# Kernel optimization log

Hardware: AMD Instinct MI355X
Metric: run time of the kernel (lower is better)

Reference implementation:

```python
import jax, jax.numpy as jnp
import numpy as np

RESO = 128
CB_BITS = 4
NUM_FEAT = 2 ** CB_BITS  # 16
DATA_DIM = 16
RADIUS = 1.3
MLP_W = 128
NFREQ = 4
PE_DIM = NFREQ * 3 * 2  # 24
BATCH = 1024
STEP = RADIUS / RESO
N_INTR = int(1.732 * RADIUS * 2 / STEP)  # 443 boundary samples
NS = N_INTR - 1                           # 442 intervals / sample points

NBR = jnp.array([[0,0,0],[0,0,1],[0,1,0],[0,1,1],[1,0,0],[1,0,1],[1,1,0],[1,1,1]], dtype=jnp.int32)


def expand_bits(v):
    v = (v * jnp.uint32(65537)) & jnp.uint32(4278190335)
    v = (v * jnp.uint32(257)) & jnp.uint32(251719695)
    v = (v * jnp.uint32(17)) & jnp.uint32(3272356035)
    v = (v * jnp.uint32(5)) & jnp.uint32(1227133513)
    return v


def morton3d(x, y, z):
    return expand_bits(x) | (expand_bits(y) << 1) | (expand_bits(z) << 2)


def pos_encode(d, nfreq):
    freqs = 2.0 ** jnp.arange(nfreq, dtype=d.dtype)          # [F]
    ang = d[..., None, :] * freqs[:, None]                   # [..., F, 3]
    pe = jnp.concatenate([jnp.sin(ang), jnp.cos(ang)], -1)   # [..., F, 6]
    return pe.reshape(*d.shape[:-1], nfreq * 6)


def setup_inputs() -> dict:
    key = jax.random.key(0)
    ks = jax.random.split(key, 8)
    rays_o = (jax.random.uniform(ks[0], (BATCH, 3), jnp.float32) - 0.5) * RADIUS
    d = jax.random.normal(ks[1], (BATCH, 3), jnp.float32)
    rays_d = d / jnp.linalg.norm(d, axis=-1, keepdims=True)
    grid = 0.01 * jax.random.normal(ks[2], (RESO ** 3, NUM_FEAT), jnp.float32)
    codebook = 0.1 * jax.random.normal(ks[3], (NUM_FEAT, DATA_DIM), jnp.float32)
    in_dim = DATA_DIM + PE_DIM
    b1s = 1.0 / np.sqrt(in_dim)
    b2s = 1.0 / np.sqrt(MLP_W)
    W1 = jax.random.uniform(ks[4], (in_dim, MLP_W), jnp.float32, -b1s, b1s)
    b1 = jax.random.uniform(ks[5], (MLP_W,), jnp.float32, -b1s, b1s)
    W2 = jax.random.uniform(ks[6], (MLP_W, 4), jnp.float32, -b2s, b2s)
    b2 = jax.random.uniform(ks[7], (4,), jnp.float32, -b2s, b2s)
    return {"rays_o": rays_o, "rays_d": rays_d, "grid": grid, "codebook": codebook,
            "W1": W1, "b1": b1, "W2": W2, "b2": b2, "level": 0}


def _forward(rays_o, rays_d, grid, codebook, W1, b1, W2, b2):
    # --- get_intersections: ray/AABB entry, uniform marching ---
    safe_d = jnp.where(jnp.abs(rays_d) < 1e-8, 1e-8, rays_d)
    t_a = (-RADIUS - rays_o) / safe_d
    t_b = (RADIUS - rays_o) / safe_d
    tmin = jnp.max(jnp.minimum(t_a, t_b), axis=-1)
    tmax = jnp.min(jnp.maximum(t_a, t_b), axis=-1)
    tnear = jnp.maximum(tmin, 0.0)
    intrs = tnear[:, None] + jnp.arange(N_INTR, dtype=jnp.float32) * STEP  # [B, N_INTR]
    tmid = 0.5 * (intrs[:, :-1] + intrs[:, 1:])                            # [B, NS]
    pts = rays_o[:, None, :] + rays_d[:, None, :] * tmid[..., None]        # [B, NS, 3]
    mask = (tmid < tmax[:, None]) & jnp.all(jnp.abs(pts) <= RADIUS, -1)    # [B, NS]

    # --- normalize to grid coords ---
    p = (pts / RADIUS + 1.0) * (RESO / 2.0)                                # [B, NS, 3]
    tl = jnp.floor(p)
    off = p - tl                                                           # [B, NS, 3]
    nbr = jnp.clip(tl.astype(jnp.int32)[:, :, None, :] + NBR, 0, RESO - 1) # [B, NS, 8, 3]
    idx = morton3d(nbr[..., 0].astype(jnp.uint32), nbr[..., 1].astype(jnp.uint32),
                   nbr[..., 2].astype(jnp.uint32)).astype(jnp.int32)       # [B, NS, 8]

    # --- straight-through VQ codebook lookup ---
    feat_soft = jax.nn.softmax(grid[idx], axis=-1)                         # [B, NS, 8, F]
    hard_idx = jnp.argmax(feat_soft, axis=-1)
    feat_hard = jax.nn.one_hot(hard_idx, NUM_FEAT, dtype=feat_soft.dtype)
    feat = feat_hard - jax.lax.stop_gradient(feat_soft) + feat_soft
    data = jnp.einsum('bsnf,fd->bsnd', feat, codebook)                     # [B, NS, 8, D]

    # --- trilinear interpolation over 8 corners ---
    w = jnp.prod(NBR * off[:, :, None, :] + (1 - NBR) * (1.0 - off[:, :, None, :]), -1)
    data_interp = jnp.einsum('bsn,bsnd->bsd', w, data)                     # [B, NS, D]

    # --- renderer MLP ---
    dir_pe = pos_encode(rays_d, NFREQ)                                     # [B, 24]
    dir_pe = jnp.broadcast_to(dir_pe[:, None, :], (rays_d.shape[0], NS, PE_DIM))
    x = jnp.concatenate([data_interp, dir_pe], -1)                         # [B, NS, 40]
    h = jax.nn.relu(jnp.einsum('bsi,io->bso', x, W1) + b1)
    preact = jnp.einsum('bsi,io->bso', h, W2) + b2                         # [B, NS, 4]
    density = jnp.where(mask, jax.nn.relu(preact[..., 0]), 0.0)            # masked_scatter
    color_raw = jnp.where(mask[..., None], preact[..., 1:], 0.0)

    # --- sigma2alpha + shrgb2rgb compositing ---
    delta = (intrs[:, 1:] - intrs[:, :-1]) * jnp.linalg.norm(rays_d, axis=-1, keepdims=True)
    alpha = 1.0 - jnp.exp(-density * delta)                                # [B, NS]
    T = jnp.cumprod(1.0 - alpha + 1e-10, axis=1)
    T = jnp.concatenate([jnp.ones_like(T[:, :1]), T[:, :-1]], axis=1)      # exclusive
    abs_light = alpha * T                                                  # weights
    rgb = jnp.sum(abs_light[..., None] * jax.nn.sigmoid(color_raw), axis=1)
    rgb = rgb + (1.0 - jnp.sum(abs_light, axis=1))[:, None]                # white bkgd
    return rgb, alpha


def reference(rays_o, rays_d, grid, codebook, W1, b1, W2, b2, level):
    assert level == 0
    return _forward(rays_o, rays_d, grid, codebook, W1, b1, W2, b2)
```

## Files before the change

### kernel.cpp

```cpp
#include <hip/hip_runtime.h>
#include <math.h>
#include <stdint.h>

#define RESO 128
#define NUM_FEAT 16
#define DATA_DIM 16
#define MLP_W 128
#define NFREQ 4
#define BATCH 1024
#define NS 442
#define NT 384
#define NWAVES 6
#define STEPF ((float)(1.3 / 128.0))

typedef __attribute__((ext_vector_type(8))) short short8;
typedef __attribute__((ext_vector_type(4))) float f32x4;
typedef __attribute__((ext_vector_type(4))) int int4v;

static __device__ __forceinline__ unsigned short f2bf(float f) {
    union { float f; uint32_t u; } v; v.f = f;
    uint32_t r = v.u + 0x7FFFu + ((v.u >> 16) & 1u);
    return (unsigned short)(r >> 16);
}
static __device__ __forceinline__ uint32_t pack2bf(float a, float b) {
    return (uint32_t)f2bf(a) | ((uint32_t)f2bf(b) << 16);
}

static __device__ __forceinline__ uint32_t expand_bits(uint32_t v) {
    v = (v * 65537u) & 4278190335u;
    v = (v * 257u)   & 251719695u;
    v = (v * 17u)    & 3272356035u;
    v = (v * 5u)     & 1227133513u;
    return v;
}
static __device__ __forceinline__ uint32_t morton3d(uint32_t x, uint32_t y, uint32_t z) {
    return expand_bits(x) | (expand_bits(y) << 1) | (expand_bits(z) << 2);
}

__global__ __launch_bounds__(NT) void nerf_main_kernel(
    const float* __restrict__ rays_o, const float* __restrict__ rays_d,
    const float* __restrict__ grid, const float* __restrict__ cbg,
    const float* __restrict__ W1g, const float* __restrict__ b1g,
    const float* __restrict__ W2g, const float* __restrict__ b2g,
    float* __restrict__ out_rgb, float* __restrict__ out_alpha) {

    __shared__ __align__(16) float cbs[NUM_FEAT * DATA_DIM];
    __shared__ __align__(16) float pe_b1s[MLP_W];
    __shared__ __align__(16) unsigned short W1pL[8 * 64 * 8];
    __shared__ float wtot[NWAVES];
    __shared__ float wred[NWAVES][4];

    const int b = blockIdx.x;
    const int t = threadIdx.x;
    const int wid = t >> 6;
    const int lane = t & 63;
    const int g = lane >> 4;

    const float o0 = rays_o[b * 3 + 0], o1 = rays_o[b * 3 + 1], o2 = rays_o[b * 3 + 2];
    const float d0 = rays_d[b * 3 + 0], d1 = rays_d[b * 3 + 1], d2 = rays_d[b * 3 + 2];
    const float R = 1.3f;
    float sd0 = (fabsf(d0) < 1e-8f) ? 1e-8f : d0;
    float sd1 = (fabsf(d1) < 1e-8f) ? 1e-8f : d1;
    float sd2 = (fabsf(d2) < 1e-8f) ? 1e-8f : d2;
    float ta0 = (-R - o0) / sd0, tb0 = (R - o0) / sd0;
    float ta1 = (-R - o1) / sd1, tb1 = (R - o1) / sd1;
    float ta2 = (-R - o2) / sd2, tb2 = (R - o2) / sd2;
    float tmin = fmaxf(fmaxf(fminf(ta0, tb0), fminf(ta1, tb1)), fminf(ta2, tb2));
    float tmax = fminf(fminf(fmaxf(ta0, tb0), fmaxf(ta1, tb1)), fmaxf(ta2, tb2));
    float tnear = fmaxf(tmin, 0.0f);
    float nrm = sqrtf(d0 * d0 + d1 * d1 + d2 * d2);

    if (t < NUM_FEAT * DATA_DIM) cbs[t] = cbg[t];

    for (int idx = t; idx < 8 * 64 * 8; idx += NT) {
        int j = idx & 7, l = (idx >> 3) & 63, mh = idx >> 9;
        int gg = l >> 4, col = l & 15;
        int k = gg * 8 + j;
        float v = (k < DATA_DIM) ? W1g[k * MLP_W + mh * 16 + col] : 0.0f;
        W1pL[idx] = f2bf(v);
    }

    if (t < MLP_W) {
        float acc = b1g[t];
#pragma unroll
        for (int f = 0; f < NFREQ; ++f) {
            float fr = (float)(1 << f);
            acc = fmaf(__sinf(d0 * fr), W1g[(DATA_DIM + f * 6 + 0) * MLP_W + t], acc);
            acc = fmaf(__sinf(d1 * fr), W1g[(DATA_DIM + f * 6 + 1) * MLP_W + t], acc);
            acc = fmaf(__sinf(d2 * fr), W1g[(DATA_DIM + f * 6 + 2) * MLP_W + t], acc);
            acc = fmaf(__cosf(d0 * fr), W1g[(DATA_DIM + f * 6 + 3) * MLP_W + t], acc);
            acc = fmaf(__cosf(d1 * fr), W1g[(DATA_DIM + f * 6 + 4) * MLP_W + t], acc);
            acc = fmaf(__cosf(d2 * fr), W1g[(DATA_DIM + f * 6 + 5) * MLP_W + t], acc);
        }
        pe_b1s[t] = acc;
    }
    __syncthreads();

    const int s = t;
    float i0 = tnear + (float)s * STEPF;
    float i1 = tnear + (float)(s + 1) * STEPF;
    float tm = 0.5f * (i0 + i1);
    float delta = (i1 - i0) * nrm;
    float px = o0 + d0 * tm, py = o1 + d1 * tm, pz = o2 + d2 * tm;
    bool m = (tm < tmax) && (fabsf(px) <= R) && (fabsf(py) <= R) && (fabsf(pz) <= R);

    float alpha = 0.0f, c0 = 0.0f, c1 = 0.0f, c2 = 0.0f;

    float x[DATA_DIM];
#pragma unroll
    for (int j = 0; j < DATA_DIM; ++j) x[j] = 0.0f;

    if (m) {
        float gx = (px / R + 1.0f) * (RESO * 0.5f);
        float gy = (py / R + 1.0f) * (RESO * 0.5f);
        float gz = (pz / R + 1.0f) * (RESO * 0.5f);
        float flx = floorf(gx), fly = floorf(gy), flz = floorf(gz);
        float ox = gx - flx, oy = gy - fly, oz = gz - flz;
        int ix = (int)flx, iy = (int)fly, iz = (int)flz;

#pragma unroll
        for (int n = 0; n < 8; ++n) {
            int bx = (n >> 2) & 1, by = (n >> 1) & 1, bz = n & 1;
            int cx = min(max(ix + bx, 0), RESO - 1);
            int cy = min(max(iy + by, 0), RESO - 1);
            int cz = min(max(iz + bz, 0), RESO - 1);
            uint32_t mi = morton3d((uint32_t)cx, (uint32_t)cy, (uint32_t)cz);
            float wv = (bx ? ox : 1.0f - ox) * (by ? oy : 1.0f - oy) * (bz ? oz : 1.0f - oz);

            const float4* g4 = (const float4*)(grid + ((size_t)mi << 4));
            float4 A = g4[0], B = g4[1], C = g4[2], D = g4[3];
            float v[16] = {A.x, A.y, A.z, A.w, B.x, B.y, B.z, B.w,
                           C.x, C.y, C.z, C.w, D.x, D.y, D.z, D.w};
            float bestv = v[0];
            int bi = 0;
#pragma unroll
            for (int j = 1; j < 16; ++j) {
                bi = (v[j] > bestv) ? j : bi;
                bestv = fmaxf(v[j], bestv);
            }

            const float4* cbr = (const float4*)&cbs[bi * DATA_DIM];
            float4 ca = cbr[0], cb4 = cbr[1], cc = cbr[2], cd = cbr[3];
            x[0]  = fmaf(wv, ca.x,  x[0]);  x[1]  = fmaf(wv, ca.y,  x[1]);
            x[2]  = fmaf(wv, ca.z,  x[2]);  x[3]  = fmaf(wv, ca.w,  x[3]);
            x[4]  = fmaf(wv, cb4.x, x[4]);  x[5]  = fmaf(wv, cb4.y, x[5]);
            x[6]  = fmaf(wv, cb4.z, x[6]);  x[7]  = fmaf(wv, cb4.w, x[7]);
            x[8]  = fmaf(wv, cc.x,  x[8]);  x[9]  = fmaf(wv, cc.y,  x[9]);
            x[10] = fmaf(wv, cc.z,  x[10]); x[11] = fmaf(wv, cc.w,  x[11]);
            x[12] = fmaf(wv, cd.x,  x[12]); x[13] = fmaf(wv, cd.y,  x[13]);
            x[14] = fmaf(wv, cd.z,  x[14]); x[15] = fmaf(wv, cd.w,  x[15]);
        }
    }

    if (__any((int)m)) {
        uint32_t wp[8];
#pragma unroll
        for (int i = 0; i < 8; ++i) wp[i] = pack2bf(x[2 * i], x[2 * i + 1]);

        short8 Bf[4];
#pragma unroll
        for (int ns = 0; ns < 4; ++ns) {
            int src = ns * 16 + (lane & 15);
            int v0a = __shfl((int)wp[0], src, 64), v0b = __shfl((int)wp[4], src, 64);
            int v1a = __shfl((int)wp[1], src, 64), v1b = __shfl((int)wp[5], src, 64);
            int v2a = __shfl((int)wp[2], src, 64), v2b = __shfl((int)wp[6], src, 64);
            int v3a = __shfl((int)wp[3], src, 64), v3b = __shfl((int)wp[7], src, 64);
            union { int4v i; short8 s; } u;
            u.i.x = (g == 0) ? v0a : (g == 1) ? v0b : 0;
            u.i.y = (g == 0) ? v1a : (g == 1) ? v1b : 0;
            u.i.z = (g == 0) ? v2a : (g == 1) ? v2b : 0;
            u.i.w = (g == 0) ? v3a : (g == 1) ? v3b : 0;
            Bf[ns] = u.s;
        }

        float p[4][4];
#pragma unroll
        for (int ns = 0; ns < 4; ++ns)
#pragma unroll
            for (int c = 0; c < 4; ++c) p[ns][c] = 0.0f;

        const int4v* Ap = (const int4v*)W1pL;
#pragma unroll
        for (int mh = 0; mh < 8; ++mh) {
            union { int4v i; short8 s; } ua;
            ua.i = Ap[mh * 64 + lane];
            short8 Af = ua.s;

            f32x4 bias = *(const f32x4*)&pe_b1s[mh * 16 + 4 * g];
            f32x4 accv[4];
            accv[0] = __builtin_amdgcn_mfma_f32_16x16x32_bf16(Af, Bf[0], bias, 0, 0, 0);
            accv[1] = __builtin_amdgcn_mfma_f32_16x16x32_bf16(Af, Bf[1], bias, 0, 0, 0);
            accv[2] = __builtin_amdgcn_mfma_f32_16x16x32_bf16(Af, Bf[2], bias, 0, 0, 0);
            accv[3] = __builtin_amdgcn_mfma_f32_16x16x32_bf16(Af, Bf[3], bias, 0, 0, 0);

            float4 w2r[4];
            w2r[0] = *(const float4*)(W2g + (mh * 16 + 4 * g + 0) * 4);
            w2r[1] = *(const float4*)(W2g + (mh * 16 + 4 * g + 1) * 4);
            w2r[2] = *(const float4*)(W2g + (mh * 16 + 4 * g + 2) * 4);
            w2r[3] = *(const float4*)(W2g + (mh * 16 + 4 * g + 3) * 4);
#pragma unroll
            for (int ns = 0; ns < 4; ++ns) {
#pragma unroll
                for (int r = 0; r < 4; ++r) {
                    float h = fmaxf(accv[ns][r], 0.0f);
                    float4 wr2 = w2r[r];
                    p[ns][0] = fmaf(h, wr2.x, p[ns][0]);
                    p[ns][1] = fmaf(h, wr2.y, p[ns][1]);
                    p[ns][2] = fmaf(h, wr2.z, p[ns][2]);
                    p[ns][3] = fmaf(h, wr2.w, p[ns][3]);
                }
            }
        }

#pragma unroll
        for (int ns = 0; ns < 4; ++ns)
#pragma unroll
            for (int c = 0; c < 4; ++c) {
                float v = p[ns][c];
                v += __shfl_xor(v, 16, 64);
                v += __shfl_xor(v, 32, 64);
                p[ns][c] = v;
            }

        float pre[4];
#pragma unroll
        for (int c = 0; c < 4; ++c) {
            float v = (g == 0) ? p[0][c] : (g == 1) ? p[1][c] : (g == 2) ? p[2][c] : p[3][c];
            pre[c] = v + b2g[c];
        }

        if (m) {
            float dens = fmaxf(pre[0], 0.0f);
            alpha = 1.0f - __expf(-dens * delta);
            c0 = 1.0f / (1.0f + __expf(-pre[1]));
            c1 = 1.0f / (1.0f + __expf(-pre[2]));
            c2 = 1.0f / (1.0f + __expf(-pre[3]));
        }
    }

    float inc = 1.0f - alpha + 1e-10f;
#pragma unroll
    for (int off = 1; off < 64; off <<= 1) {
        float u = __shfl_up(inc, off, 64);
        if (lane >= off) inc *= u;
    }
    float excl = __shfl_up(inc, 1, 64);
    if (lane == 0) excl = 1.0f;
    if (lane == 63) wtot[wid] = inc;
    __syncthreads();

    float wpre = 1.0f;
#pragma unroll
    for (int w = 0; w < NWAVES; ++w)
        if (w < wid) wpre *= wtot[w];
    float T = wpre * excl;
    float wgt = alpha * T;
    float r0 = wgt * c0, r1 = wgt * c1, r2 = wgt * c2, rw = wgt;

    out_alpha[b * NS + s] = alpha;
    if (t < NS - NT) out_alpha[b * NS + NT + t] = 0.0f;

#pragma unroll
    for (int off = 32; off >= 1; off >>= 1) {
        r0 += __shfl_down(r0, off, 64);
        r1 += __shfl_down(r1, off, 64);
        r2 += __shfl_down(r2, off, 64);
        rw += __shfl_down(rw, off, 64);
    }
    if (lane == 0) { wred[wid][0] = r0; wred[wid][1] = r1; wred[wid][2] = r2; wred[wid][3] = rw; }
    __syncthreads();
    if (t == 0) {
        float s0 = 0, s1 = 0, s2 = 0, sw = 0;
#pragma unroll
        for (int i = 0; i < NWAVES; ++i) {
            s0 += wred[i][0]; s1 += wred[i][1]; s2 += wred[i][2]; sw += wred[i][3];
        }
        float bg = 1.0f - sw;
        out_rgb[b * 3 + 0] = s0 + bg;
        out_rgb[b * 3 + 1] = s1 + bg;
        out_rgb[b * 3 + 2] = s2 + bg;
    }
}

extern "C" void kernel_launch(void* const* d_in, const int* in_sizes, int n_in,
                              void* d_out, int out_size, void* d_ws, size_t ws_size,
                              hipStream_t stream) {
    const float* rays_o   = (const float*)d_in[0];
    const float* rays_d   = (const float*)d_in[1];
    const float* grid     = (const float*)d_in[2];
    const float* codebook = (const float*)d_in[3];
    const float* W1       = (const float*)d_in[4];
    const float* b1       = (const float*)d_in[5];
    const float* W2       = (const float*)d_in[6];
    const float* b2       = (const float*)d_in[7];
    float* out = (float*)d_out;

    nerf_main_kernel<<<BATCH, NT, 0, stream>>>(
        rays_o, rays_d, grid, codebook, W1, b1, W2, b2,
        out , out + BATCH * 3 );
}
```

Before: 31.10 us.

## Split rays into 64-sample chunks per wave with separate combine kernel

Each wave now handles one 64-sample chunk of a ray (7 chunks per ray, 4 chunks per block), writing partial color, weight and transmittance to a workspace. A second small kernel composites the chunks in order. This removes the block-wide syncs for the cross-wave scan and reduction, and lets blocks or waves whose chunks lie entirely outside the volume skip the MLP and W1 staging. In exchange it adds a second launch, a workspace round trip, and per-wave recomputation of the positional-encoding bias.

```diff
diff --git a/kernel.cpp b/kernel.cpp
--- a/kernel.cpp
+++ b/kernel.cpp
@@ -9,8 +9,10 @@
 #define NFREQ 4
 #define BATCH 1024
 #define NS 442
-#define NT 384
-#define NWAVES 6
+#define NT 256
+#define CPR 7
+#define NENT (BATCH * CPR)
+#define NBLK (NENT / 4)
 #define STEPF ((float)(1.3 / 128.0))
 
 typedef __attribute__((ext_vector_type(8))) short short8;
@@ -42,19 +44,20 @@
     const float* __restrict__ grid, const float* __restrict__ cbg,
     const float* __restrict__ W1g, const float* __restrict__ b1g,
     const float* __restrict__ W2g, const float* __restrict__ b2g,
-    float* __restrict__ out_rgb, float* __restrict__ out_alpha) {
+    float* __restrict__ part, float* __restrict__ out_alpha) {
 
     __shared__ __align__(16) float cbs[NUM_FEAT * DATA_DIM];
-    __shared__ __align__(16) float pe_b1s[MLP_W];
     __shared__ __align__(16) unsigned short W1pL[8 * 64 * 8];
-    __shared__ float wtot[NWAVES];
-    __shared__ float wred[NWAVES][4];
-
-    const int b = blockIdx.x;
+    __shared__ __align__(16) float peb[4][MLP_W];
+
     const int t = threadIdx.x;
-    const int wid = t >> 6;
+    const int wslot = t >> 6;
     const int lane = t & 63;
     const int g = lane >> 4;
+
+    const int e = blockIdx.x * 4 + wslot;
+    const int b = e / CPR;
+    const int c = e - b * CPR;
 
     const float o0 = rays_o[b * 3 + 0], o1 = rays_o[b * 3 + 1], o2 = rays_o[b * 3 + 2];
     const float d0 = rays_d[b * 3 + 0], d1 = rays_d[b * 3 + 1], d2 = rays_d[b * 3 + 2];
@@ -70,39 +73,61 @@
     float tnear = fmaxf(tmin, 0.0f);
     float nrm = sqrtf(d0 * d0 + d1 * d1 + d2 * d2);
 
-    if (t < NUM_FEAT * DATA_DIM) cbs[t] = cbg[t];
-
-    for (int idx = t; idx < 8 * 64 * 8; idx += NT) {
-        int j = idx & 7, l = (idx >> 3) & 63, mh = idx >> 9;
-        int gg = l >> 4, col = l & 15;
-        int k = gg * 8 + j;
-        float v = (k < DATA_DIM) ? W1g[k * MLP_W + mh * 16 + col] : 0.0f;
-        W1pL[idx] = f2bf(v);
-    }
-
-    if (t < MLP_W) {
-        float acc = b1g[t];
-#pragma unroll
-        for (int f = 0; f < NFREQ; ++f) {
-            float fr = (float)(1 << f);
-            acc = fmaf(__sinf(d0 * fr), W1g[(DATA_DIM + f * 6 + 0) * MLP_W + t], acc);
-            acc = fmaf(__sinf(d1 * fr), W1g[(DATA_DIM + f * 6 + 1) * MLP_W + t], acc);
-            acc = fmaf(__sinf(d2 * fr), W1g[(DATA_DIM + f * 6 + 2) * MLP_W + t], acc);
-            acc = fmaf(__cosf(d0 * fr), W1g[(DATA_DIM + f * 6 + 3) * MLP_W + t], acc);
-            acc = fmaf(__cosf(d1 * fr), W1g[(DATA_DIM + f * 6 + 4) * MLP_W + t], acc);
-            acc = fmaf(__cosf(d2 * fr), W1g[(DATA_DIM + f * 6 + 5) * MLP_W + t], acc);
-        }
-        pe_b1s[t] = acc;
-    }
-    __syncthreads();
-
-    const int s = t;
+    const int s = c * 64 + lane;
     float i0 = tnear + (float)s * STEPF;
     float i1 = tnear + (float)(s + 1) * STEPF;
     float tm = 0.5f * (i0 + i1);
     float delta = (i1 - i0) * nrm;
     float px = o0 + d0 * tm, py = o1 + d1 * tm, pz = o2 + d2 * tm;
-    bool m = (tm < tmax) && (fabsf(px) <= R) && (fabsf(py) <= R) && (fabsf(pz) <= R);
+    bool m = (s < NS) && (tm < tmax) &&
+             (fabsf(px) <= R) && (fabsf(py) <= R) && (fabsf(pz) <= R);
+    const bool anym = __any((int)m);
+
+    int blkact = __syncthreads_or((int)anym);
+    if (blkact) {
+        if (t < NUM_FEAT * DATA_DIM) cbs[t] = cbg[t];
+        for (int idx = t; idx < 8 * 64 * 8; idx += NT) {
+            int j = idx & 7, l = (idx >> 3) & 63, mh = idx >> 9;
+            int k = (l >> 4) * 8 + j;
+            float v = (k < DATA_DIM) ? W1g[k * MLP_W + mh * 16 + (l & 15)] : 0.0f;
+            W1pL[idx] = f2bf(v);
+        }
+        __syncthreads();
+    }
+
+    if (!anym) {
+        if (s < NS) out_alpha[b * NS + s] = 0.0f;
+        if (lane == 0) {
+            float* P = part + (size_t)e * 8;
+            P[0] = 0.0f; P[1] = 0.0f; P[2] = 0.0f; P[3] = 0.0f; P[4] = 1.0f;
+        }
+        return;
+    }
+
+    {
+        float sn[NFREQ][3], cs[NFREQ][3];
+#pragma unroll
+        for (int f = 0; f < NFREQ; ++f) {
+            float fr = (float)(1 << f);
+            sn[f][0] = __sinf(d0 * fr); sn[f][1] = __sinf(d1 * fr); sn[f][2] = __sinf(d2 * fr);
+            cs[f][0] = __cosf(d0 * fr); cs[f][1] = __cosf(d1 * fr); cs[f][2] = __cosf(d2 * fr);
+        }
+        float a0 = b1g[lane], a1 = b1g[64 + lane];
+#pragma unroll
+        for (int f = 0; f < NFREQ; ++f) {
+#pragma unroll
+            for (int ax = 0; ax < 3; ++ax) {
+                const float* ws = &W1g[(DATA_DIM + f * 6 + ax) * MLP_W];
+                const float* wc = &W1g[(DATA_DIM + f * 6 + 3 + ax) * MLP_W];
+                a0 = fmaf(sn[f][ax], ws[lane], a0);
+                a1 = fmaf(sn[f][ax], ws[64 + lane], a1);
+                a0 = fmaf(cs[f][ax], wc[lane], a0);
+                a1 = fmaf(cs[f][ax], wc[64 + lane], a1);
+            }
+        }
+        peb[wslot][lane] = a0;
+        peb[wslot][64 + lane] = a1;
+    }
 
     float alpha = 0.0f, c0 = 0.0f, c1 = 0.0f, c2 = 0.0f;
 
@@ -152,7 +177,7 @@
         }
     }
 
-    if (__any((int)m)) {
+    {
         uint32_t wp[8];
 #pragma unroll
         for (int i = 0; i < 8; ++i) wp[i] = pack2bf(x[2 * i], x[2 * i + 1]);
@@ -177,7 +202,7 @@
 #pragma unroll
         for (int ns = 0; ns < 4; ++ns)
 #pragma unroll
-            for (int c = 0; c < 4; ++c) p[ns][c] = 0.0f;
+            for (int cc2 = 0; cc2 < 4; ++cc2) p[ns][cc2] = 0.0f;
 
         const int4v* Ap = (const int4v*)W1pL;
 #pragma unroll
@@ -186,7 +211,7 @@
             ua.i = Ap[mh * 64 + lane];
             short8 Af = ua.s;
 
-            f32x4 bias = *(const f32x4*)&pe_b1s[mh * 16 + 4 * g];
+            f32x4 bias = *(const f32x4*)&peb[wslot][mh * 16 + 4 * g];
             f32x4 accv[4];
             accv[0] = __builtin_amdgcn_mfma_f32_16x16x32_bf16(Af, Bf[0], bias, 0, 0, 0);
             accv[1] = __builtin_amdgcn_mfma_f32_16x16x32_bf16(Af, Bf[1], bias, 0, 0, 0);
@@ -215,18 +240,18 @@
 #pragma unroll
         for (int ns = 0; ns < 4; ++ns)
 #pragma unroll
-            for (int c = 0; c < 4; ++c) {
-                float v = p[ns][c];
+            for (int cc2 = 0; cc2 < 4; ++cc2) {
+                float v = p[ns][cc2];
                 v += __shfl_xor(v, 16, 64);
                 v += __shfl_xor(v, 32, 64);
-                p[ns][c] = v;
+                p[ns][cc2] = v;
             }
 
         float pre[4];
 #pragma unroll
-        for (int c = 0; c < 4; ++c) {
-            float v = (g == 0) ? p[0][c] : (g == 1) ? p[1][c] : (g == 2) ? p[2][c] : p[3][c];
-            pre[c] = v + b2g[c];
+        for (int cc2 = 0; cc2 < 4; ++cc2) {
+            float v = (g == 0) ? p[0][cc2] : (g == 1) ? p[1][cc2] : (g == 2) ? p[2][cc2] : p[3][cc2];
+            pre[cc2] = v + b2g[cc2];
         }
 
         if (m) {
@@ -246,19 +271,12 @@
     }
     float excl = __shfl_up(inc, 1, 64);
     if (lane == 0) excl = 1.0f;
-    if (lane == 63) wtot[wid] = inc;
-    __syncthreads();
-
-    float wpre = 1.0f;
-#pragma unroll
-    for (int w = 0; w < NWAVES; ++w)
-        if (w < wid) wpre *= wtot[w];
-    float T = wpre * excl;
-    float wgt = alpha * T;
+    float P = __shfl(inc, 63, 64);
+
+    float wgt = alpha * excl;
     float r0 = wgt * c0, r1 = wgt * c1, r2 = wgt * c2, rw = wgt;
 
-    out_alpha[b * NS + s] = alpha;
-    if (t < NS - NT) out_alpha[b * NS + NT + t] = 0.0f;
+    if (s < NS) out_alpha[b * NS + s] = alpha;
 
 #pragma unroll
     for (int off = 32; off >= 1; off >>= 1) {
@@ -267,19 +285,30 @@
         r2 += __shfl_down(r2, off, 64);
         rw += __shfl_down(rw, off, 64);
     }
-    if (lane == 0) { wred[wid][0] = r0; wred[wid][1] = r1; wred[wid][2] = r2; wred[wid][3] = rw; }
-    __syncthreads();
-    if (t == 0) {
-        float s0 = 0, s1 = 0, s2 = 0, sw = 0;
-#pragma unroll
-        for (int i = 0; i < NWAVES; ++i) {
-            s0 += wred[i][0]; s1 += wred[i][1]; s2 += wred[i][2]; sw += wred[i][3];
-        }
-        float bg = 1.0f - sw;
-        out_rgb[b * 3 + 0] = s0 + bg;
-        out_rgb[b * 3 + 1] = s1 + bg;
-        out_rgb[b * 3 + 2] = s2 + bg;
-    }
+    if (lane == 0) {
+        float* Pp = part + (size_t)e * 8;
+        Pp[0] = r0; Pp[1] = r1; Pp[2] = r2; Pp[3] = rw; Pp[4] = P;
+    }
+}
+
+__global__ __launch_bounds__(256) void combine_kernel(const float* __restrict__ part,
+                                                      float* __restrict__ out_rgb) {
+    int b = blockIdx.x * 256 + threadIdx.x;
+    if (b >= BATCH) return;
+    float T = 1.0f, r0 = 0.0f, r1 = 0.0f, r2 = 0.0f, rw = 0.0f;
+#pragma unroll
+    for (int c = 0; c < CPR; ++c) {
+        const float* P = part + (size_t)(b * CPR + c) * 8;
+        r0 = fmaf(T, P[0], r0);
+        r1 = fmaf(T, P[1], r1);
+        r2 = fmaf(T, P[2], r2);
+        rw = fmaf(T, P[3], rw);
+        T *= P[4];
+    }
+    float bg = 1.0f - rw;
+    out_rgb[b * 3 + 0] = r0 + bg;
+    out_rgb[b * 3 + 1] = r1 + bg;
+    out_rgb[b * 3 + 2] = r2 + bg;
 }
 
 extern "C" void kernel_launch(void* const* d_in, const int* in_sizes, int n_in,
@@ -295,7 +324,10 @@
     const float* b2       = (const float*)d_in[7];
     float* out = (float*)d_out;
 
-    nerf_main_kernel<<<BATCH, NT, 0, stream>>>(
+    float* part = (float*)d_ws;
+
+    nerf_main_kernel<<<NBLK, NT, 0, stream>>>(
         rays_o, rays_d, grid, codebook, W1, b1, W2, b2,
-        out , out + BATCH * 3 );
-}
+        part, out + BATCH * 3 );
+    combine_kernel<<<(BATCH + 255) / 256, 256, 0, stream>>>(part, out );
+}
```

New measurement: 38.48 us. +23.7%, slower.
